# Optimization experiments

Hardware: AMD Instinct MI355X
Metric: run time of the kernel (lower is better)

The kernel has to match this reference:

```python
import jax, jax.numpy as jnp
import numpy as np

# YOLOv1 config constants
GRIDS = 7
CLASSES = 20
IMAGE_SIZE = 448.0
LAMBDA_COOR = 5.0
LAMBDA_NOOBJ = 0.5
FEAT = 5 + CLASSES  # 25


def _make_target(bboxes):
    """bboxes: (B, n, 5) pixel coords [x1,y1,x2,y2,label] -> target (B,G,G,25).
    First-write-wins per grid cell, matching the torch per-box loop."""
    B, n, _ = bboxes.shape
    box = bboxes[..., :4] / IMAGE_SIZE                      # (B,n,4) in [0,1]
    label = bboxes[..., 4].astype(jnp.int32)                # (B,n)
    xc = (box[..., 0] + box[..., 2]) * 0.5
    yc = (box[..., 1] + box[..., 3]) * 0.5
    w = box[..., 2] - box[..., 0]
    h = box[..., 3] - box[..., 1]
    xg = jnp.floor(xc * GRIDS).astype(jnp.int32)
    yg = jnp.floor(yc * GRIDS).astype(jnp.int32)
    xo = xc * GRIDS - xg
    yo = yc * GRIDS - yg
    cell = yg * GRIDS + xg                                  # (B,n) flat cell id
    # first-come-first-serve: drop box j if an earlier box k<j hit the same cell
    same = cell[:, :, None] == cell[:, None, :]             # (B,n,n)
    earlier = jnp.tril(jnp.ones((n, n), dtype=bool), k=-1)
    keep = ~jnp.any(same & earlier, axis=-1)                # (B,n)
    one_hot = jax.nn.one_hot(label, CLASSES, dtype=jnp.float32)
    vals = jnp.concatenate(
        [xo[..., None], yo[..., None], w[..., None], h[..., None],
         jnp.ones_like(xo)[..., None], one_hot], axis=-1)   # (B,n,25)
    # route dropped boxes to an out-of-range index -> scatter drops them;
    # kept boxes have unique cells per image so .set is deterministic
    flat_idx = jnp.arange(B, dtype=jnp.int32)[:, None] * (GRIDS * GRIDS) + cell
    flat_idx = jnp.where(keep, flat_idx, B * GRIDS * GRIDS)  # OOB sentinel
    target = jnp.zeros((B * GRIDS * GRIDS, FEAT), dtype=jnp.float32)
    target = target.at[flat_idx.reshape(-1)].set(
        vals.reshape(-1, FEAT), mode='drop')
    return target.reshape(B, GRIDS, GRIDS, FEAT)


def reference(pred, bboxes):
    target = _make_target(bboxes)
    obj_mask = target[:, :, :, 4]
    noobj_mask = (1.0 - obj_mask) * LAMBDA_NOOBJ
    loss_contain = (target[:, :, :, 4] - pred[:, :, :, 4]) ** 2
    loss_contain = ((obj_mask + noobj_mask) * loss_contain).sum((1, 2))
    loss_coord = ((target[:, :, :, 0] - pred[:, :, :, 0]) ** 2
                  + (target[:, :, :, 1] - pred[:, :, :, 1]) ** 2
                  + (jnp.sqrt(target[:, :, :, 2]) - jnp.sqrt(pred[:, :, :, 2])) ** 2
                  + (jnp.sqrt(target[:, :, :, 3]) - jnp.sqrt(pred[:, :, :, 3])) ** 2)
    loss_coord = (obj_mask * loss_coord * LAMBDA_COOR).sum((1, 2))
    loss_class = (target[:, :, :, 5:] - pred[:, :, :, 5:]) ** 2
    loss_class = (obj_mask[..., None] * loss_class).sum((1, 2, 3))
    return (loss_contain + loss_coord + loss_class).mean()


def setup_inputs() -> dict:
    key = jax.random.key(0)
    k1, k2, k3, k4, k5 = jax.random.split(key, 5)
    B, n = 16384, 8
    # pred in (0.05, 0.95) so sqrt of w/h channels is well-defined
    pred = jax.random.uniform(k1, (B, GRIDS, GRIDS, FEAT), dtype=jnp.float32) * 0.9 + 0.05
    # valid boxes in pixels: centers in (0.25,0.75)*448, sizes in (0.05,0.4)*448
    cx = (jax.random.uniform(k2, (B, n)) * 0.5 + 0.25) * IMAGE_SIZE
    cy = (jax.random.uniform(k3, (B, n)) * 0.5 + 0.25) * IMAGE_SIZE
    wh = (jax.random.uniform(k4, (B, n, 2)) * 0.35 + 0.05) * IMAGE_SIZE
    x1 = cx - wh[..., 0] * 0.5
    x2 = cx + wh[..., 0] * 0.5
    y1 = cy - wh[..., 1] * 0.5
    y2 = cy + wh[..., 1] * 0.5
    label = jax.random.randint(k5, (B, n), 0, CLASSES).astype(jnp.float32)
    bboxes = jnp.stack([x1, y1, x2, y2, label], axis=-1).astype(jnp.float32)
    return {"pred": pred, "bboxes": bboxes}
```

## Files before the change

kernel.cpp:

```cpp
#include <hip/hip_runtime.h>

#define GRIDS 7
#define NCELL 49
#define NFEAT 25
#define CELLSZ 1225
#define BPB 16
#define MAXBOX 16


__global__ __launch_bounds__(256) void yolo_main(
    const float* __restrict__ pred, const float* __restrict__ bbox,
    float* __restrict__ partial, int B, int nbox)
{
    __shared__ float sBox[BPB * MAXBOX * 5];
    __shared__ int   sOff[BPB * MAXBOX];
    __shared__ int   sKeep[BPB * MAXBOX];
    __shared__ float sRed[4];

    const int tid = threadIdx.x;
    const long long b0 = (long long)blockIdx.x * BPB;
    const int nb = min(BPB, B - (int)b0);
    const int nbx = nb * nbox;
    const float* pb = pred + b0 * CELLSZ;

    const int ncells = nb * NCELL;
    float cf0 = 0.f, cf1 = 0.f, cf2 = 0.f, cf3 = 0.f;
    {
        int t0 = tid, t1 = tid + 256, t2 = tid + 512, t3 = tid + 768;
        if (t0 < ncells) {
            unsigned lb = ((unsigned)t0 * 2676u) >> 17;
            cf0 = pb[lb * CELLSZ + ((unsigned)t0 - lb * 49u) * NFEAT + 4];
        }
        if (t1 < ncells) {
            unsigned lb = ((unsigned)t1 * 2676u) >> 17;
            cf1 = pb[lb * CELLSZ + ((unsigned)t1 - lb * 49u) * NFEAT + 4];
        }
        if (t2 < ncells) {
            unsigned lb = ((unsigned)t2 * 2676u) >> 17;
            cf2 = pb[lb * CELLSZ + ((unsigned)t2 - lb * 49u) * NFEAT + 4];
        }
        if (t3 < ncells) {
            unsigned lb = ((unsigned)t3 * 2676u) >> 17;
            cf3 = pb[lb * CELLSZ + ((unsigned)t3 - lb * 49u) * NFEAT + 4];
        }
    }

    if (tid < nbx) {
        const float* bx = bbox + (b0 * nbox + tid) * 5;
        float x1 = bx[0] / 448.f, y1 = bx[1] / 448.f;
        float x2 = bx[2] / 448.f, y2 = bx[3] / 448.f;
        float xc = (x1 + x2) * 0.5f, yc = (y1 + y2) * 0.5f;
        float w  = x2 - x1,          h  = y2 - y1;
        float xs = xc * (float)GRIDS, ys = yc * (float)GRIDS;
        float xg = floorf(xs), yg = floorf(ys);
        int lb = tid / nbox;
        int cell = (int)yg * GRIDS + (int)xg;
        sOff[tid] = lb * CELLSZ + cell * NFEAT;
        float* e = &sBox[tid * 5];
        e[0] = xs - xg; e[1] = ys - yg;
        e[2] = sqrtf(w); e[3] = sqrtf(h);
        e[4] = bx[4];
    }
    __syncthreads();

    if (tid < nbx) {
        int lb = tid / nbox;
        int o  = sOff[tid];
        int k = 1;
        for (int j = lb * nbox; j < tid; ++j)
            if (sOff[j] == o) { k = 0; break; }
        sKeep[tid] = k;
    }
    __syncthreads();

    const int wid = tid >> 6, lane = tid & 63;
    const int f = lane & 31;
    const int cbase = wid * 2 + (lane >> 5);
    float gv[16];
    #pragma unroll
    for (int k = 0; k < 16; ++k) {
        int bi = cbase + 8 * k;
        bool v = (bi < nbx) && (f < NFEAT) && sKeep[bi];
        gv[k] = v ? pb[sOff[bi] + f] : 0.f;
    }

    float acc = 0.f;
    acc = fmaf(0.5f * cf0, cf0, acc);
    acc = fmaf(0.5f * cf1, cf1, acc);
    acc = fmaf(0.5f * cf2, cf2, acc);
    acc = fmaf(0.5f * cf3, cf3, acc);

    #pragma unroll
    for (int k = 0; k < 16; ++k) {
        int bi = cbase + 8 * k;
        bool v = (bi < nbx) && (f < NFEAT) && sKeep[bi];
        if (v) {
            const float* e = &sBox[bi * 5];
            float p = gv[k];
            float term;
            if (f == 4) {
                float d = 1.f - p;
                term = fmaf(d, d, -0.5f * p * p);
            } else if (f < 4) {
                float q = (f >= 2) ? sqrtf(p) : p;
                float d = e[f] - q;
                term = 5.f * d * d;
            } else {
                float t = ((int)e[4] == f - 5) ? 1.f : 0.f;
                float d = t - p;
                term = d * d;
            }
            acc += term;
        }
    }
    for (int bi = 128 + cbase; bi < nbx; bi += 8) {
        if (f < NFEAT && sKeep[bi]) {
            const float* e = &sBox[bi * 5];
            float p = pb[sOff[bi] + f];
            float term;
            if (f == 4) {
                float d = 1.f - p;
                term = fmaf(d, d, -0.5f * p * p);
            } else if (f < 4) {
                float q = (f >= 2) ? sqrtf(p) : p;
                float d = e[f] - q;
                term = 5.f * d * d;
            } else {
                float t = ((int)e[4] == f - 5) ? 1.f : 0.f;
                float d = t - p;
                term = d * d;
            }
            acc += term;
        }
    }

    for (int off = 32; off; off >>= 1)
        acc += __shfl_down(acc, off, 64);
    if ((tid & 63) == 0) sRed[tid >> 6] = acc;
    __syncthreads();
    if (tid == 0)
        partial[blockIdx.x] = sRed[0] + sRed[1] + sRed[2] + sRed[3];
}

__global__ __launch_bounds__(256) void yolo_reduce(
    const float* __restrict__ partial, int n, float* __restrict__ out, int B)
{
    __shared__ double s[256];
    const float4* p4 = (const float4*)partial;
    const int n4 = n >> 2;
    double a = 0.0;
    for (int j = threadIdx.x; j < n4; j += 256) {
        float4 v = p4[j];
        a += (double)v.x + (double)v.y + (double)v.z + (double)v.w;
    }
    for (int j = (n4 << 2) + threadIdx.x; j < n; j += 256)
        a += (double)partial[j];
    s[threadIdx.x] = a;
    __syncthreads();
    for (int str = 128; str; str >>= 1) {
        if (threadIdx.x < str) s[threadIdx.x] += s[threadIdx.x + str];
        __syncthreads();
    }
    if (threadIdx.x == 0) out[0] = (float)(s[0] / (double)B);
}

extern "C" void kernel_launch(void* const* d_in, const int* in_sizes, int n_in,
                              void* d_out, int out_size, void* d_ws, size_t ws_size,
                              hipStream_t stream) {
    const float* pred = (const float*)d_in[0];
    const float* bbox = (const float*)d_in[1];
    int B = in_sizes[0] / CELLSZ;
    int nbox = in_sizes[1] / (B * 5);
    if (nbox > MAXBOX) nbox = MAXBOX;
    float* out = (float*)d_out;
    float* partial = (float*)d_ws;

    int nblocks = (B + BPB - 1) / BPB;
    yolo_main<<<nblocks, 256, 0, stream>>>(pred, bbox, partial, B, nbox);
    yolo_reduce<<<1, 256, 0, stream>>>(partial, nblocks, out, B);
}
```

Before: 26.32 us.

## Fuse final reduction into main kernel via hierarchical last-block atomic counters

```diff
diff --git a/kernel.cpp b/kernel.cpp
--- a/kernel.cpp
+++ b/kernel.cpp
@@ -8,14 +8,18 @@
 #define MAXBOX 16
 
 
-__global__ __launch_bounds__(256) void yolo_main(
+__global__ __launch_bounds__(256) void yolo_onek(
     const float* __restrict__ pred, const float* __restrict__ bbox,
-    float* __restrict__ partial, int B, int nbox)
+    float* __restrict__ partial, unsigned* __restrict__ gcnt,
+    unsigned* __restrict__ root, float* __restrict__ out,
+    int B, int nbox, int nblocks, int ngroups)
 {
-    __shared__ float sBox[BPB * MAXBOX * 5];
-    __shared__ int   sOff[BPB * MAXBOX];
-    __shared__ int   sKeep[BPB * MAXBOX];
-    __shared__ float sRed[4];
+    __shared__ float  sBox[BPB * MAXBOX * 5];
+    __shared__ int    sOff[BPB * MAXBOX];
+    __shared__ int    sKeep[BPB * MAXBOX];
+    __shared__ float  sRed[4];
+    __shared__ double sRedD[256];
+    __shared__ int    sLast;
 
     const int tid = threadIdx.x;
     const long long b0 = (long long)blockIdx.x * BPB;
@@ -138,30 +142,39 @@
         acc += __shfl_down(acc, off, 64);
     if ((tid & 63) == 0) sRed[tid >> 6] = acc;
     __syncthreads();
-    if (tid == 0)
-        partial[blockIdx.x] = sRed[0] + sRed[1] + sRed[2] + sRed[3];
-}
-
-__global__ __launch_bounds__(256) void yolo_reduce(
-    const float* __restrict__ partial, int n, float* __restrict__ out, int B)
-{
-    __shared__ double s[256];
-    const float4* p4 = (const float4*)partial;
-    const int n4 = n >> 2;
-    double a = 0.0;
-    for (int j = threadIdx.x; j < n4; j += 256) {
-        float4 v = p4[j];
-        a += (double)v.x + (double)v.y + (double)v.z + (double)v.w;
-    }
-    for (int j = (n4 << 2) + threadIdx.x; j < n; j += 256)
-        a += (double)partial[j];
-    s[threadIdx.x] = a;
-    __syncthreads();
-    for (int str = 128; str; str >>= 1) {
-        if (threadIdx.x < str) s[threadIdx.x] += s[threadIdx.x + str];
+
+    if (tid == 0) {
+        float bsum = sRed[0] + sRed[1] + sRed[2] + sRed[3];
+        __hip_atomic_store(&partial[blockIdx.x], bsum, __ATOMIC_RELAXED,
+                           __HIP_MEMORY_SCOPE_AGENT);
+        asm volatile("s_waitcnt vmcnt(0)" ::: "memory");
+        int g = blockIdx.x >> 5;
+        int gsz = min(32, nblocks - (g << 5));
+        int last = 0;
+        unsigned gp = __hip_atomic_fetch_add(&gcnt[g * 16], 1u, __ATOMIC_RELAXED,
+                                             __HIP_MEMORY_SCOPE_AGENT);
+        if ((int)gp == gsz - 1) {
+            unsigned rp = __hip_atomic_fetch_add(root, 1u, __ATOMIC_RELAXED,
+                                                 __HIP_MEMORY_SCOPE_AGENT);
+            last = ((int)rp == ngroups - 1);
+        }
+        sLast = last;
+    }
+    __syncthreads();
+
+    if (sLast) {
+        double a = 0.0;
+        for (int j = tid; j < nblocks; j += 256)
+            a += (double)__hip_atomic_load(&partial[j], __ATOMIC_RELAXED,
+                                           __HIP_MEMORY_SCOPE_AGENT);
+        sRedD[tid] = a;
         __syncthreads();
-    }
-    if (threadIdx.x == 0) out[0] = (float)(s[0] / (double)B);
+        for (int s = 128; s; s >>= 1) {
+            if (tid < s) sRedD[tid] += sRedD[tid + s];
+            __syncthreads();
+        }
+        if (tid == 0) out[0] = (float)(sRedD[0] / (double)B);
+    }
 }
 
 extern "C" void kernel_launch(void* const* d_in, const int* in_sizes, int n_in,
@@ -173,9 +186,15 @@
     int nbox = in_sizes[1] / (B * 5);
     if (nbox > MAXBOX) nbox = MAXBOX;
     float* out = (float*)d_out;
+
+    int nblocks = (B + BPB - 1) / BPB;
+    int ngroups = (nblocks + 31) / 32;
+
     float* partial = (float*)d_ws;
-
-    int nblocks = (B + BPB - 1) / BPB;
-    yolo_main<<<nblocks, 256, 0, stream>>>(pred, bbox, partial, B, nbox);
-    yolo_reduce<<<1, 256, 0, stream>>>(partial, nblocks, out, B);
+    unsigned* gcnt = (unsigned*)((char*)d_ws + 65536);
+    unsigned* root = (unsigned*)((char*)d_ws + 65536 + 128 * 64);
+
+    hipMemsetAsync((char*)d_ws + 65536, 0, 128 * 64 + 64, stream);
+    yolo_onek<<<nblocks, 256, 0, stream>>>(pred, bbox, partial, gcnt, root, out,
+                                           B, nbox, nblocks, ngroups);
 }
```

After: 31.84 us. 21.0% more time.
